# Kernel tuning notes

Hardware: AMD Instinct MI355X
Metric: run time of the kernel (lower is better)

The kernel has to match this reference:

```python
import jax, jax.numpy as jnp
import numpy as np

B = 2048   # number of samples; acts as seq_len for the (S,N,E) transformer
DIN = 768
D = 512    # hidden_dim
H = 8      # nheads
HD = D // H
L = 3      # encoder layers
P = 40     # num_prototypes
Q = D // 4 # 128, projected feature dim
EPS = 1e-5


def setup_inputs() -> dict:
    key = jax.random.key(0)
    ks = jax.random.split(key, 22)
    s = 0.02
    rn = lambda k, shape: jax.random.normal(k, shape, jnp.float32) * s
    return {
        "x": jax.random.normal(ks[0], (B, DIN), jnp.float32),
        "reduce_w": rn(ks[1], (D, DIN)), "reduce_b": rn(ks[2], (D,)),
        "in_w": rn(ks[3], (L, 3 * D, D)), "in_b": rn(ks[4], (L, 3 * D)),
        "out_w": rn(ks[5], (L, D, D)), "out_b": rn(ks[6], (L, D)),
        "ff1_w": rn(ks[7], (L, D, D)), "ff1_b": rn(ks[8], (L, D)),
        "ff2_w": rn(ks[9], (L, D, D)), "ff2_b": rn(ks[10], (L, D)),
        "ln1_w": jnp.ones((L, D), jnp.float32), "ln1_b": jnp.zeros((L, D), jnp.float32),
        "ln2_w": jnp.ones((L, D), jnp.float32), "ln2_b": jnp.zeros((L, D), jnp.float32),
        "mlp_w1": rn(ks[11], (D, D)), "mlp_b1": rn(ks[12], (D,)),
        "mlp_w2": rn(ks[13], (D, D)), "mlp_b2": rn(ks[14], (D,)),
        "mlp_w3": rn(ks[15], (Q, D)), "mlp_b3": rn(ks[16], (Q,)),
        "highlights": jax.random.normal(ks[17], (P, Q), jnp.float32),
        "negatives": jax.random.normal(ks[18], (P, Q), jnp.float32),
    }


def _inorm(x):
    # InstanceNorm1d (affine=False) on a 2D tensor: per-row normalize over last dim
    m = x.mean(-1, keepdims=True)
    v = ((x - m) ** 2).mean(-1, keepdims=True)  # biased variance, matches torch
    return (x - m) * jax.lax.rsqrt(v + EPS)


def _ln(x, w, b):
    m = x.mean(-1, keepdims=True)
    v = ((x - m) ** 2).mean(-1, keepdims=True)
    return (x - m) * jax.lax.rsqrt(v + EPS) * w + b


def _cdist(a, cb):
    # euclidean distances [B,P]
    d2 = (a * a).sum(-1, keepdims=True) + (cb * cb).sum(-1) - 2.0 * a @ cb.T
    return jnp.sqrt(jnp.maximum(d2, 0.0))


def reference(x, reduce_w, reduce_b, in_w, in_b, out_w, out_b,
              ff1_w, ff1_b, ff2_w, ff2_b, ln1_w, ln1_b, ln2_w, ln2_b,
              mlp_w1, mlp_b1, mlp_w2, mlp_b2, mlp_w3, mlp_b3,
              highlights, negatives):
    feat0 = _inorm(x @ reduce_w.T + reduce_b)  # [B,D]

    # TransformerEncoder, post-norm, relu FFN, dropout off (eval).
    # Input is (seq=B, batch=1, D) -> attention across all B rows.
    feat = feat0
    scale = 1.0 / np.sqrt(HD)
    for i in range(L):
        qkv = feat @ in_w[i].T + in_b[i]           # [B,3D]
        q, k, v = jnp.split(qkv, 3, axis=-1)
        q = q.reshape(B, H, HD)
        k = k.reshape(B, H, HD)
        v = v.reshape(B, H, HD)
        scores = jnp.einsum('ihd,jhd->hij', q, k) * scale  # [H,B,B]
        attn = jax.nn.softmax(scores, axis=-1)
        ctx = jnp.einsum('hij,jhd->ihd', attn, v).reshape(B, D)
        attn_out = ctx @ out_w[i].T + out_b[i]
        feat = _ln(feat + attn_out, ln1_w[i], ln1_b[i])
        ff = jax.nn.relu(feat @ ff1_w[i].T + ff1_b[i]) @ ff2_w[i].T + ff2_b[i]
        feat = _ln(feat + ff, ln2_w[i], ln2_b[i])

    feat = feat0 + _inorm(feat)

    # MLP 512 -> 512 -> 512 -> 128 (relu on all but last)
    feat = jax.nn.relu(feat @ mlp_w1.T + mlp_b1)
    feat = jax.nn.relu(feat @ mlp_w2.T + mlp_b2)
    feat = feat @ mlp_w3.T + mlp_b3
    feat = _inorm(feat)  # [B,Q]

    positive_dist = _cdist(feat, highlights).min(-1)
    negative_dist = _cdist(feat, negatives).min(-1)
    logits = jnp.stack([-negative_dist, -positive_dist], axis=-1)  # [B,2]
    return logits
```

## Files before the change

### kernel.cpp

```cpp
#include <hip/hip_runtime.h>
#include <math.h>
#include <cstddef>

#define EPS 1e-5f

typedef __attribute__((ext_vector_type(8))) short bf16x8;
typedef __attribute__((ext_vector_type(4))) float f32x4;

__device__ __forceinline__ float wave_sum(float v) {
#pragma unroll
  for (int o = 32; o > 0; o >>= 1) v += __shfl_xor(v, o, 64);
  return v;
}

__device__ __forceinline__ unsigned short f2b(float f) {
  union { float f; unsigned int u; } v; v.f = f;
  unsigned int r = (v.u + 0x7FFFu + ((v.u >> 16) & 1u)) >> 16;
  return (unsigned short)r;
}
__device__ __forceinline__ float b2f(unsigned short u) {
  union { unsigned int u; float f; } v; v.u = ((unsigned int)u) << 16;
  return v.f;
}

struct WConvArgs {
  const float* src[8];
  unsigned short* dst[8];
  int n[8];
};
__global__ __launch_bounds__(256) void conv_w(WConvArgs a) {
  const int arr = blockIdx.y;
  const int i = (blockIdx.x * 256 + threadIdx.x) * 4;
  if (i >= a.n[arr]) return;
  const float4 f = *(const float4*)(a.src[arr] + i);
  unsigned short t[4] = {f2b(f.x), f2b(f.y), f2b(f.z), f2b(f.w)};
  unsigned short* d = a.dst[arr] + i;
  *(ushort2*)d = *(ushort2*)&t[0];
  *(ushort2*)(d + 2) = *(ushort2*)&t[2];
}

template <int RELU, int AF32, int OUT_F32, int OUT_BF16, int MERGE>
__global__ __launch_bounds__(256) void gemm32(
    const void* __restrict__ Aptr, const float* __restrict__ pmp,
    const unsigned short* __restrict__ W, const float* __restrict__ bias,
    float* __restrict__ Cf, unsigned short* __restrict__ Cb,
    int M, int N, int K) {
  __shared__ __align__(16) unsigned short As[2][32][72];
  __shared__ __align__(16) unsigned short Ws[2][64][72];
  const int tid = threadIdx.x;
  const int wid = tid >> 6, lane = tid & 63;
  const int ln = lane & 15, quad = lane >> 4;
  const int m0 = blockIdx.x * 32, n0 = blockIdx.y * 64;
  const int arow = tid >> 3, aseg = tid & 7;
  const int wrow = tid >> 2, wseg = tid & 3;
  const int KS = K >> 6;

  bf16x8 ra;
  float4 ra32[2];
  bf16x8 rwb0, rwb1;
  bf16x8 rp0, rp1;
  float rl0, rl1;

  auto load_tile = [&](int ks) {
    const int k0 = ks * 64;
    if (MERGE) {
      const int h = ks;
      const int row = m0 + arow;
      const size_t b0 = (size_t)(h * 2048 + row);
      const size_t b1 = (size_t)((8 + h) * 2048 + row);
      rl0 = pmp[b0]; rl1 = pmp[b1];
      rp0 = *(const bf16x8*)((const unsigned short*)Aptr + b0 * 64 + aseg * 8);
      rp1 = *(const bf16x8*)((const unsigned short*)Aptr + b1 * 64 + aseg * 8);
    } else if (AF32) {
      const float* ap = (const float*)Aptr + (size_t)(m0 + arow) * K + k0 + aseg * 8;
      ra32[0] = *(const float4*)ap;
      ra32[1] = *(const float4*)(ap + 4);
    } else {
      ra = *(const bf16x8*)((const unsigned short*)Aptr +
                            (size_t)(m0 + arow) * K + k0 + aseg * 8);
    }
    const unsigned short* wp = W + (size_t)(n0 + wrow) * K + k0 + wseg * 16;
    rwb0 = *(const bf16x8*)wp;
    rwb1 = *(const bf16x8*)(wp + 8);
  };

  auto store_tile = [&](int buf) {
    if (MERGE) {
      float inv = 1.f / (rl0 + rl1);
      unsigned short ta[8];
#pragma unroll
      for (int j = 0; j < 8; ++j)
        ta[j] = f2b(inv * (b2f((unsigned short)rp0[j]) +
                           b2f((unsigned short)rp1[j])));
      *(bf16x8*)&As[buf][arow][aseg * 8] = *(const bf16x8*)&ta[0];
    } else if (AF32) {
      unsigned short ta[8];
      ta[0] = f2b(ra32[0].x); ta[1] = f2b(ra32[0].y);
      ta[2] = f2b(ra32[0].z); ta[3] = f2b(ra32[0].w);
      ta[4] = f2b(ra32[1].x); ta[5] = f2b(ra32[1].y);
      ta[6] = f2b(ra32[1].z); ta[7] = f2b(ra32[1].w);
      *(bf16x8*)&As[buf][arow][aseg * 8] = *(const bf16x8*)&ta[0];
    } else {
      *(bf16x8*)&As[buf][arow][aseg * 8] = ra;
    }
    *(bf16x8*)&Ws[buf][wrow][wseg * 16] = rwb0;
    *(bf16x8*)&Ws[buf][wrow][wseg * 16 + 8] = rwb1;
  };

  f32x4 acc[2];
  acc[0] = (f32x4){0.f, 0.f, 0.f, 0.f};
  acc[1] = (f32x4){0.f, 0.f, 0.f, 0.f};

  const int mrow = (wid & 1) * 16, nh = wid >> 1;

  load_tile(0);
  store_tile(0);
  __syncthreads();

#pragma unroll 1
  for (int ks = 0; ks < KS; ++ks) {
    const int cur = ks & 1;
    if (ks + 1 < KS) load_tile(ks + 1);
#pragma unroll
    for (int kc = 0; kc < 2; ++kc) {
      bf16x8 af = *(const bf16x8*)&As[cur][mrow + ln][kc * 32 + quad * 8];
#pragma unroll
      for (int nt = 0; nt < 2; ++nt) {
        bf16x8 wf = *(const bf16x8*)&Ws[cur][nh * 32 + nt * 16 + ln][kc * 32 + quad * 8];
        acc[nt] = __builtin_amdgcn_mfma_f32_16x16x32_bf16(af, wf, acc[nt], 0, 0, 0);
      }
    }
    if (ks + 1 < KS) store_tile(cur ^ 1);
    __syncthreads();
  }

  const int gm = m0 + mrow + quad * 4;
#pragma unroll
  for (int nt = 0; nt < 2; ++nt) {
    const int gn = n0 + nh * 32 + nt * 16 + ln;
    float bv = bias[gn];
#pragma unroll
    for (int r = 0; r < 4; ++r) {
      float v = acc[nt][r] + bv;
      if (RELU) v = fmaxf(v, 0.f);
      if (OUT_F32) Cf[(size_t)(gm + r) * N + gn] = v;
      if (OUT_BF16) Cb[(size_t)(gm + r) * N + gn] = f2b(v);
    }
  }
}

__global__ __launch_bounds__(256) void flash_attn6(
    const unsigned short* __restrict__ qkv, float* __restrict__ pm,
    unsigned short* __restrict__ po) {
  __shared__ __align__(16) unsigned short Ks[2][64][72];
  __shared__ __align__(16) unsigned short Vt[2][64][72];
  __shared__ __align__(16) unsigned short Ps[64][72];
  const int qt = blockIdx.x, h = blockIdx.y, sp = blockIdx.z;
  const int tid = threadIdx.x;
  const int wid = tid >> 6, lane = tid & 63;
  const int ln = lane & 15, quad = lane >> 4;
  const int wq0 = wid * 16;

  bf16x8 aq[2];
  {
    const unsigned short* qp =
        qkv + (size_t)(qt * 64 + wq0 + ln) * 1536 + h * 64 + quad * 8;
    aq[0] = *(const bf16x8*)qp;
    aq[1] = *(const bf16x8*)(qp + 32);
  }

  const int key = tid >> 2, seg = tid & 3;
  bf16x8 rk0, rk1;
  unsigned short tv[16];

  auto load_kv = [&](int t) {
    const int g = sp * 16 + t;
    const unsigned short* kr =
        qkv + (size_t)(g * 64 + key) * 1536 + 512 + h * 64 + seg * 16;
    rk0 = *(const bf16x8*)kr;
    rk1 = *(const bf16x8*)(kr + 8);
#pragma unroll
    for (int j = 0; j < 16; ++j)
      tv[j] = qkv[(size_t)(g * 64 + wid * 16 + j) * 1536 + 1024 + h * 64 + lane];
  };
  auto store_kv = [&](int buf) {
    *(bf16x8*)&Ks[buf][key][seg * 16] = rk0;
    *(bf16x8*)&Ks[buf][key][seg * 16 + 8] = rk1;
    *(bf16x8*)&Vt[buf][lane][wid * 16] = *(const bf16x8*)&tv[0];
    *(bf16x8*)&Vt[buf][lane][wid * 16 + 8] = *(const bf16x8*)&tv[8];
  };

  float l_r[4] = {0.f, 0.f, 0.f, 0.f};
  f32x4 acc_o[4];
#pragma unroll
  for (int nt = 0; nt < 4; ++nt) acc_o[nt] = (f32x4){0.f, 0.f, 0.f, 0.f};

  load_kv(0);
  store_kv(0);
  __syncthreads();

#pragma unroll 1
  for (int t = 0; t < 16; ++t) {
    const int cur = t & 1;
    if (t + 1 < 16) load_kv(t + 1);

    f32x4 s_acc[4];
#pragma unroll
    for (int nt = 0; nt < 4; ++nt) s_acc[nt] = (f32x4){0.f, 0.f, 0.f, 0.f};
#pragma unroll
    for (int nt = 0; nt < 4; ++nt) {
      bf16x8 kf0 = *(const bf16x8*)&Ks[cur][nt * 16 + ln][quad * 8];
      bf16x8 kf1 = *(const bf16x8*)&Ks[cur][nt * 16 + ln][32 + quad * 8];
      s_acc[nt] = __builtin_amdgcn_mfma_f32_16x16x32_bf16(aq[0], kf0, s_acc[nt], 0, 0, 0);
      s_acc[nt] = __builtin_amdgcn_mfma_f32_16x16x32_bf16(aq[1], kf1, s_acc[nt], 0, 0, 0);
    }

#pragma unroll
    for (int nt = 0; nt < 4; ++nt) {
#pragma unroll
      for (int r = 0; r < 4; ++r) {
        float p = __expf(s_acc[nt][r] * 0.125f);
        l_r[r] += p;
        Ps[wq0 + quad * 4 + r][nt * 16 + ln] = f2b(p);
      }
    }

#pragma unroll
    for (int kc = 0; kc < 2; ++kc) {
      bf16x8 pf = *(const bf16x8*)&Ps[wq0 + ln][kc * 32 + quad * 8];
#pragma unroll
      for (int nt = 0; nt < 4; ++nt) {
        bf16x8 vf = *(const bf16x8*)&Vt[cur][nt * 16 + ln][kc * 32 + quad * 8];
        acc_o[nt] = __builtin_amdgcn_mfma_f32_16x16x32_bf16(pf, vf, acc_o[nt], 0, 0, 0);
      }
    }
    if (t + 1 < 16) store_kv(cur ^ 1);
    __syncthreads();
  }

  const size_t base = (size_t)((sp * 8 + h) * 2048 + qt * 64);
#pragma unroll
  for (int r = 0; r < 4; ++r) {
    float l = l_r[r];
    l += __shfl_xor(l, 1, 64);
    l += __shfl_xor(l, 2, 64);
    l += __shfl_xor(l, 4, 64);
    l += __shfl_xor(l, 8, 64);
    const size_t row = base + wq0 + quad * 4 + r;
    if (ln == 0) pm[row] = l;
#pragma unroll
    for (int nt = 0; nt < 4; ++nt)
      po[row * 64 + nt * 16 + ln] = f2b(acc_o[nt][r]);
  }
}

__global__ __launch_bounds__(256) void inorm512(float* __restrict__ dst,
                                                unsigned short* __restrict__ dstb,
                                                const float* __restrict__ src) {
  const int row = blockIdx.x * 4 + (threadIdx.x >> 6);
  const int lane = threadIdx.x & 63;
  const float4* s = (const float4*)(src + (size_t)row * 512);
  float4 a = s[lane], b = s[lane + 64];
  float sum = a.x + a.y + a.z + a.w + b.x + b.y + b.z + b.w;
  float mean = wave_sum(sum) * (1.f / 512.f);
  float vs = (a.x - mean) * (a.x - mean) + (a.y - mean) * (a.y - mean) +
             (a.z - mean) * (a.z - mean) + (a.w - mean) * (a.w - mean) +
             (b.x - mean) * (b.x - mean) + (b.y - mean) * (b.y - mean) +
             (b.z - mean) * (b.z - mean) + (b.w - mean) * (b.w - mean);
  float rs = rsqrtf(wave_sum(vs) * (1.f / 512.f) + EPS);
  float4 oa, obv;
  oa.x = (a.x - mean) * rs; oa.y = (a.y - mean) * rs;
  oa.z = (a.z - mean) * rs; oa.w = (a.w - mean) * rs;
  obv.x = (b.x - mean) * rs; obv.y = (b.y - mean) * rs;
  obv.z = (b.z - mean) * rs; obv.w = (b.w - mean) * rs;
  float4* d = (float4*)(dst + (size_t)row * 512);
  d[lane] = oa; d[lane + 64] = obv;
  unsigned short* db = dstb + (size_t)row * 512;
  unsigned short t0[4] = {f2b(oa.x), f2b(oa.y), f2b(oa.z), f2b(oa.w)};
  unsigned short t1[4] = {f2b(obv.x), f2b(obv.y), f2b(obv.z), f2b(obv.w)};
  *(ushort2*)&db[lane * 4] = *(ushort2*)&t0[0];
  *(ushort2*)&db[lane * 4 + 2] = *(ushort2*)&t0[2];
  *(ushort2*)&db[256 + lane * 4] = *(ushort2*)&t1[0];
  *(ushort2*)&db[256 + lane * 4 + 2] = *(ushort2*)&t1[2];
}

__global__ __launch_bounds__(256) void ln_res(float* __restrict__ dst,
                                              unsigned short* __restrict__ dstb,
                                              const float* __restrict__ xsrc,
                                              const float* __restrict__ delta,
                                              const float* __restrict__ w,
                                              const float* __restrict__ bb) {
  const int row = blockIdx.x * 4 + (threadIdx.x >> 6);
  const int lane = threadIdx.x & 63;
  const float4* xs = (const float4*)(xsrc + (size_t)row * 512);
  const float4* dl = (const float4*)(delta + (size_t)row * 512);
  float4 a = xs[lane], b = xs[lane + 64];
  float4 da = dl[lane], db4 = dl[lane + 64];
  a.x += da.x; a.y += da.y; a.z += da.z; a.w += da.w;
  b.x += db4.x; b.y += db4.y; b.z += db4.z; b.w += db4.w;
  float sum = a.x + a.y + a.z + a.w + b.x + b.y + b.z + b.w;
  float mean = wave_sum(sum) * (1.f / 512.f);
  float vs = (a.x - mean) * (a.x - mean) + (a.y - mean) * (a.y - mean) +
             (a.z - mean) * (a.z - mean) + (a.w - mean) * (a.w - mean) +
             (b.x - mean) * (b.x - mean) + (b.y - mean) * (b.y - mean) +
             (b.z - mean) * (b.z - mean) + (b.w - mean) * (b.w - mean);
  float rs = rsqrtf(wave_sum(vs) * (1.f / 512.f) + EPS);
  float4 wa = ((const float4*)w)[lane], wb = ((const float4*)w)[lane + 64];
  float4 ba = ((const float4*)bb)[lane], bbv = ((const float4*)bb)[lane + 64];
  float4 oa, ob2;
  oa.x = (a.x - mean) * rs * wa.x + ba.x; oa.y = (a.y - mean) * rs * wa.y + ba.y;
  oa.z = (a.z - mean) * rs * wa.z + ba.z; oa.w = (a.w - mean) * rs * wa.w + ba.w;
  ob2.x = (b.x - mean) * rs * wb.x + bbv.x; ob2.y = (b.y - mean) * rs * wb.y + bbv.y;
  ob2.z = (b.z - mean) * rs * wb.z + bbv.z; ob2.w = (b.w - mean) * rs * wb.w + bbv.w;
  float4* d = (float4*)(dst + (size_t)row * 512);
  d[lane] = oa; d[lane + 64] = ob2;
  unsigned short* dbp = dstb + (size_t)row * 512;
  unsigned short t0[4] = {f2b(oa.x), f2b(oa.y), f2b(oa.z), f2b(oa.w)};
  unsigned short t1[4] = {f2b(ob2.x), f2b(ob2.y), f2b(ob2.z), f2b(ob2.w)};
  *(ushort2*)&dbp[lane * 4] = *(ushort2*)&t0[0];
  *(ushort2*)&dbp[lane * 4 + 2] = *(ushort2*)&t0[2];
  *(ushort2*)&dbp[256 + lane * 4] = *(ushort2*)&t1[0];
  *(ushort2*)&dbp[256 + lane * 4 + 2] = *(ushort2*)&t1[2];
}

__global__ __launch_bounds__(256) void add_inorm(float* __restrict__ feat,
                                                 unsigned short* __restrict__ featb,
                                                 const float* __restrict__ feat0) {
  const int row = blockIdx.x * 4 + (threadIdx.x >> 6);
  const int lane = threadIdx.x & 63;
  float4* f = (float4*)(feat + (size_t)row * 512);
  const float4* f0 = (const float4*)(feat0 + (size_t)row * 512);
  float4 a = f[lane], b = f[lane + 64];
  float sum = a.x + a.y + a.z + a.w + b.x + b.y + b.z + b.w;
  float mean = wave_sum(sum) * (1.f / 512.f);
  float vs = (a.x - mean) * (a.x - mean) + (a.y - mean) * (a.y - mean) +
             (a.z - mean) * (a.z - mean) + (a.w - mean) * (a.w - mean) +
             (b.x - mean) * (b.x - mean) + (b.y - mean) * (b.y - mean) +
             (b.z - mean) * (b.z - mean) + (b.w - mean) * (b.w - mean);
  float rs = rsqrtf(wave_sum(vs) * (1.f / 512.f) + EPS);
  float4 za = f0[lane], zb = f0[lane + 64];
  float4 oa, ob2;
  oa.x = za.x + (a.x - mean) * rs; oa.y = za.y + (a.y - mean) * rs;
  oa.z = za.z + (a.z - mean) * rs; oa.w = za.w + (a.w - mean) * rs;
  ob2.x = zb.x + (b.x - mean) * rs; ob2.y = zb.y + (b.y - mean) * rs;
  ob2.z = zb.z + (b.z - mean) * rs; ob2.w = zb.w + (b.w - mean) * rs;
  f[lane] = oa; f[lane + 64] = ob2;
  unsigned short* dbp = featb + (size_t)row * 512;
  unsigned short t0[4] = {f2b(oa.x), f2b(oa.y), f2b(oa.z), f2b(oa.w)};
  unsigned short t1[4] = {f2b(ob2.x), f2b(ob2.y), f2b(ob2.z), f2b(ob2.w)};
  *(ushort2*)&dbp[lane * 4] = *(ushort2*)&t0[0];
  *(ushort2*)&dbp[lane * 4 + 2] = *(ushort2*)&t0[2];
  *(ushort2*)&dbp[256 + lane * 4] = *(ushort2*)&t1[0];
  *(ushort2*)&dbp[256 + lane * 4 + 2] = *(ushort2*)&t1[2];
}

__global__ __launch_bounds__(256) void dist2(const float* __restrict__ fq,
                                             const float* __restrict__ hi,
                                             const float* __restrict__ ne,
                                             float* __restrict__ out) {
  const int row = blockIdx.x * 4 + (threadIdx.x >> 6);
  const int lane = threadIdx.x & 63;
  float f0 = fq[(size_t)row * 128 + lane];
  float f1 = fq[(size_t)row * 128 + 64 + lane];
  float mean = wave_sum(f0 + f1) * (1.f / 128.f);
  float vs = (f0 - mean) * (f0 - mean) + (f1 - mean) * (f1 - mean);
  float rs = rsqrtf(wave_sum(vs) * (1.f / 128.f) + EPS);
  f0 = (f0 - mean) * rs;
  f1 = (f1 - mean) * rs;
  float mp = 1e30f, mn = 1e30f;
  for (int p = 0; p < 40; ++p) {
    float h0 = hi[p * 128 + lane], h1 = hi[p * 128 + 64 + lane];
    float d0 = f0 - h0, d1 = f1 - h1;
    float d2 = wave_sum(d0 * d0 + d1 * d1);
    mp = fminf(mp, d2);
    float n0 = ne[p * 128 + lane], n1 = ne[p * 128 + 64 + lane];
    d0 = f0 - n0; d1 = f1 - n1;
    d2 = wave_sum(d0 * d0 + d1 * d1);
    mn = fminf(mn, d2);
  }
  if (lane == 0) {
    out[row * 2 + 0] = -sqrtf(mn);
    out[row * 2 + 1] = -sqrtf(mp);
  }
}

extern "C" void kernel_launch(void* const* d_in, const int* in_sizes, int n_in,
                              void* d_out, int out_size, void* d_ws, size_t ws_size,
                              hipStream_t stream) {
  const float* x        = (const float*)d_in[0];
  const float* reduce_w = (const float*)d_in[1];
  const float* reduce_b = (const float*)d_in[2];
  const float* in_w     = (const float*)d_in[3];
  const float* in_b     = (const float*)d_in[4];
  const float* out_w    = (const float*)d_in[5];
  const float* out_b    = (const float*)d_in[6];
  const float* ff1_w    = (const float*)d_in[7];
  const float* ff1_b    = (const float*)d_in[8];
  const float* ff2_w    = (const float*)d_in[9];
  const float* ff2_b    = (const float*)d_in[10];
  const float* ln1_w    = (const float*)d_in[11];
  const float* ln1_b    = (const float*)d_in[12];
  const float* ln2_w    = (const float*)d_in[13];
  const float* ln2_b    = (const float*)d_in[14];
  const float* mlp_w1   = (const float*)d_in[15];
  const float* mlp_b1   = (const float*)d_in[16];
  const float* mlp_w2   = (const float*)d_in[17];
  const float* mlp_b2   = (const float*)d_in[18];
  const float* mlp_w3   = (const float*)d_in[19];
  const float* mlp_b3   = (const float*)d_in[20];
  const float* hi       = (const float*)d_in[21];
  const float* ne       = (const float*)d_in[22];
  float* out = (float*)d_out;
  float* ws = (float*)d_ws;

  const size_t MD = (size_t)2048 * 512;
  float* feat0_f = ws;
  float* feat_f  = ws + MD;
  float* tmp_f   = ws + 2 * MD;
  float* pm      = ws + 3 * MD;
  unsigned short* u = (unsigned short*)(ws + 3 * MD + 32768);
  unsigned short* qkv_b   = u;
  unsigned short* feat0_b = u + 3 * MD;
  unsigned short* feat_b  = u + 4 * MD;
  unsigned short* relu_b  = u + 5 * MD;
  unsigned short* po_b    = u + 6 * MD;
  unsigned short* relu2_b = qkv_b;
  float* featq_f = tmp_f;

  unsigned short* wb = u + 8 * MD;
  unsigned short* reduce_wb = wb;
  unsigned short* in_wb     = wb + 393216;
  unsigned short* out_wb    = in_wb + 2359296;
  unsigned short* ff1_wb    = out_wb + 786432;
  unsigned short* ff2_wb    = ff1_wb + 786432;
  unsigned short* mlp_w1b   = ff2_wb + 786432;
  unsigned short* mlp_w2b   = mlp_w1b + 262144;
  unsigned short* mlp_w3b   = mlp_w2b + 262144;

  dim3 blk(256);
  WConvArgs wa;
  wa.src[0] = reduce_w; wa.dst[0] = reduce_wb; wa.n[0] = 393216;
  wa.src[1] = in_w;     wa.dst[1] = in_wb;     wa.n[1] = 2359296;
  wa.src[2] = out_w;    wa.dst[2] = out_wb;    wa.n[2] = 786432;
  wa.src[3] = ff1_w;    wa.dst[3] = ff1_wb;    wa.n[3] = 786432;
  wa.src[4] = ff2_w;    wa.dst[4] = ff2_wb;    wa.n[4] = 786432;
  wa.src[5] = mlp_w1;   wa.dst[5] = mlp_w1b;   wa.n[5] = 262144;
  wa.src[6] = mlp_w2;   wa.dst[6] = mlp_w2b;   wa.n[6] = 262144;
  wa.src[7] = mlp_w3;   wa.dst[7] = mlp_w3b;   wa.n[7] = 65536;
  conv_w<<<dim3(2304, 8), blk, 0, stream>>>(wa);

  gemm32<0, 1, 1, 0, 0><<<dim3(64, 8), blk, 0, stream>>>(
      x, nullptr, reduce_wb, reduce_b, feat0_f, nullptr, 2048, 512, 768);
  inorm512<<<512, blk, 0, stream>>>(feat0_f, feat0_b, feat0_f);

  for (int i = 0; i < 3; ++i) {
    const float* fin_f = (i == 0) ? feat0_f : feat_f;
    const unsigned short* fin_b = (i == 0) ? feat0_b : feat_b;
    gemm32<0, 0, 0, 1, 0><<<dim3(64, 24), blk, 0, stream>>>(
        fin_b, nullptr, in_wb + (size_t)i * 1536 * 512, in_b + i * 1536,
        nullptr, qkv_b, 2048, 1536, 512);
    flash_attn6<<<dim3(32, 8, 2), blk, 0, stream>>>(qkv_b, pm, po_b);
    gemm32<0, 0, 1, 0, 1><<<dim3(64, 8), blk, 0, stream>>>(
        po_b, pm, out_wb + (size_t)i * 512 * 512, out_b + i * 512,
        tmp_f, nullptr, 2048, 512, 512);
    ln_res<<<512, blk, 0, stream>>>(feat_f, feat_b, fin_f, tmp_f,
                                    ln1_w + i * 512, ln1_b + i * 512);
    gemm32<1, 0, 0, 1, 0><<<dim3(64, 8), blk, 0, stream>>>(
        feat_b, nullptr, ff1_wb + (size_t)i * 512 * 512, ff1_b + i * 512,
        nullptr, relu_b, 2048, 512, 512);
    gemm32<0, 0, 1, 0, 0><<<dim3(64, 8), blk, 0, stream>>>(
        relu_b, nullptr, ff2_wb + (size_t)i * 512 * 512, ff2_b + i * 512,
        tmp_f, nullptr, 2048, 512, 512);
    ln_res<<<512, blk, 0, stream>>>(feat_f, feat_b, feat_f, tmp_f,
                                    ln2_w + i * 512, ln2_b + i * 512);
  }

  add_inorm<<<512, blk, 0, stream>>>(feat_f, feat_b, feat0_f);
  gemm32<1, 0, 0, 1, 0><<<dim3(64, 8), blk, 0, stream>>>(
      feat_b, nullptr, mlp_w1b, mlp_b1, nullptr, relu_b, 2048, 512, 512);
  gemm32<1, 0, 0, 1, 0><<<dim3(64, 8), blk, 0, stream>>>(
      relu_b, nullptr, mlp_w2b, mlp_b2, nullptr, relu2_b, 2048, 512, 512);
  gemm32<0, 0, 1, 0, 0><<<dim3(64, 2), blk, 0, stream>>>(
      relu2_b, nullptr, mlp_w3b, mlp_b3, featq_f, nullptr, 2048, 128, 512);
  dist2<<<512, blk, 0, stream>>>(featq_f, hi, ne, out);
}
```

Before: 373.1 us.

## Split attention keys four ways, fold Q scaling and residual adds into GEMMs

The flash attention grid grows from 2 to 4 key splits, each processing 8 key tiles. The K/V shared buffers become single-buffered with an extra barrier per tile, and the out-projection merge step now sums four partials. The 1/sqrt(d) query scaling moves into the QKV GEMM epilogue. The residual additions move into the out-proj and FF2 GEMM epilogues, so the layernorm kernels read one tensor instead of two. This aims to raise attention occupancy across CUs and cut memory traffic, at the cost of more partial-result traffic and extra synchronization inside the attention loop.

```diff
diff --git a/kernel.cpp b/kernel.cpp
--- a/kernel.cpp
+++ b/kernel.cpp
@@ -39,12 +39,13 @@
   *(ushort2*)(d + 2) = *(ushort2*)&t[2];
 }
 
-template <int RELU, int AF32, int OUT_F32, int OUT_BF16, int MERGE>
+template <int RELU, int AF32, int OUT_F32, int OUT_BF16, int MERGE, int RESID,
+          int SCALEQ>
 __global__ __launch_bounds__(256) void gemm32(
     const void* __restrict__ Aptr, const float* __restrict__ pmp,
     const unsigned short* __restrict__ W, const float* __restrict__ bias,
-    float* __restrict__ Cf, unsigned short* __restrict__ Cb,
-    int M, int N, int K) {
+    const float* __restrict__ Rf, float* __restrict__ Cf,
+    unsigned short* __restrict__ Cb, int M, int N, int K) {
   __shared__ __align__(16) unsigned short As[2][32][72];
   __shared__ __align__(16) unsigned short Ws[2][64][72];
   const int tid = threadIdx.x;
@@ -58,19 +59,21 @@
   bf16x8 ra;
   float4 ra32[2];
   bf16x8 rwb0, rwb1;
-  bf16x8 rp0, rp1;
-  float rl0, rl1;
+  bf16x8 rp[4];
+  float rl;
 
   auto load_tile = [&](int ks) {
     const int k0 = ks * 64;
     if (MERGE) {
       const int h = ks;
       const int row = m0 + arow;
-      const size_t b0 = (size_t)(h * 2048 + row);
-      const size_t b1 = (size_t)((8 + h) * 2048 + row);
-      rl0 = pmp[b0]; rl1 = pmp[b1];
-      rp0 = *(const bf16x8*)((const unsigned short*)Aptr + b0 * 64 + aseg * 8);
-      rp1 = *(const bf16x8*)((const unsigned short*)Aptr + b1 * 64 + aseg * 8);
+      rl = 0.f;
+#pragma unroll
+      for (int s = 0; s < 4; ++s) {
+        const size_t b = (size_t)((s * 8 + h) * 2048 + row);
+        rl += pmp[b];
+        rp[s] = *(const bf16x8*)((const unsigned short*)Aptr + b * 64 + aseg * 8);
+      }
     } else if (AF32) {
       const float* ap = (const float*)Aptr + (size_t)(m0 + arow) * K + k0 + aseg * 8;
       ra32[0] = *(const float4*)ap;
@@ -86,12 +89,14 @@
 
   auto store_tile = [&](int buf) {
     if (MERGE) {
-      float inv = 1.f / (rl0 + rl1);
+      float inv = 1.f / rl;
       unsigned short ta[8];
 #pragma unroll
-      for (int j = 0; j < 8; ++j)
-        ta[j] = f2b(inv * (b2f((unsigned short)rp0[j]) +
-                           b2f((unsigned short)rp1[j])));
+      for (int j = 0; j < 8; ++j) {
+        float s = b2f((unsigned short)rp[0][j]) + b2f((unsigned short)rp[1][j]) +
+                  b2f((unsigned short)rp[2][j]) + b2f((unsigned short)rp[3][j]);
+        ta[j] = f2b(inv * s);
+      }
       *(bf16x8*)&As[buf][arow][aseg * 8] = *(const bf16x8*)&ta[0];
     } else if (AF32) {
       unsigned short ta[8];
@@ -135,6 +140,7 @@
   }
 
   const int gm = m0 + mrow + quad * 4;
+  const float qs = (SCALEQ && n0 < 512) ? 0.125f : 1.f;
 #pragma unroll
   for (int nt = 0; nt < 2; ++nt) {
     const int gn = n0 + nh * 32 + nt * 16 + ln;
@@ -142,18 +148,20 @@
 #pragma unroll
     for (int r = 0; r < 4; ++r) {
       float v = acc[nt][r] + bv;
+      if (SCALEQ) v *= qs;
       if (RELU) v = fmaxf(v, 0.f);
+      if (RESID) v += Rf[(size_t)(gm + r) * N + gn];
       if (OUT_F32) Cf[(size_t)(gm + r) * N + gn] = v;
       if (OUT_BF16) Cb[(size_t)(gm + r) * N + gn] = f2b(v);
     }
   }
 }
 
-__global__ __launch_bounds__(256) void flash_attn6(
+__global__ __launch_bounds__(256) void flash_attn7(
     const unsigned short* __restrict__ qkv, float* __restrict__ pm,
     unsigned short* __restrict__ po) {
-  __shared__ __align__(16) unsigned short Ks[2][64][72];
-  __shared__ __align__(16) unsigned short Vt[2][64][72];
+  __shared__ __align__(16) unsigned short Ks[64][72];
+  __shared__ __align__(16) unsigned short Vt[64][72];
   __shared__ __align__(16) unsigned short Ps[64][72];
   const int qt = blockIdx.x, h = blockIdx.y, sp = blockIdx.z;
   const int tid = threadIdx.x;
@@ -174,7 +182,7 @@
   unsigned short tv[16];
 
   auto load_kv = [&](int t) {
-    const int g = sp * 16 + t;
+    const int g = sp * 8 + t;
     const unsigned short* kr =
         qkv + (size_t)(g * 64 + key) * 1536 + 512 + h * 64 + seg * 16;
     rk0 = *(const bf16x8*)kr;
@@ -183,11 +191,11 @@
     for (int j = 0; j < 16; ++j)
       tv[j] = qkv[(size_t)(g * 64 + wid * 16 + j) * 1536 + 1024 + h * 64 + lane];
   };
-  auto store_kv = [&](int buf) {
-    *(bf16x8*)&Ks[buf][key][seg * 16] = rk0;
-    *(bf16x8*)&Ks[buf][key][seg * 16 + 8] = rk1;
-    *(bf16x8*)&Vt[buf][lane][wid * 16] = *(const bf16x8*)&tv[0];
-    *(bf16x8*)&Vt[buf][lane][wid * 16 + 8] = *(const bf16x8*)&tv[8];
+  auto store_kv = [&]() {
+    *(bf16x8*)&Ks[key][seg * 16] = rk0;
+    *(bf16x8*)&Ks[key][seg * 16 + 8] = rk1;
+    *(bf16x8*)&Vt[lane][wid * 16] = *(const bf16x8*)&tv[0];
+    *(bf16x8*)&Vt[lane][wid * 16 + 8] = *(const bf16x8*)&tv[8];
   };
 
   float l_r[4] = {0.f, 0.f, 0.f, 0.f};
@@ -196,21 +204,20 @@
   for (int nt = 0; nt < 4; ++nt) acc_o[nt] = (f32x4){0.f, 0.f, 0.f, 0.f};
 
   load_kv(0);
-  store_kv(0);
+  store_kv();
   __syncthreads();
 
 #pragma unroll 1
-  for (int t = 0; t < 16; ++t) {
-    const int cur = t & 1;
-    if (t + 1 < 16) load_kv(t + 1);
+  for (int t = 0; t < 8; ++t) {
+    if (t + 1 < 8) load_kv(t + 1);
 
     f32x4 s_acc[4];
 #pragma unroll
     for (int nt = 0; nt < 4; ++nt) s_acc[nt] = (f32x4){0.f, 0.f, 0.f, 0.f};
 #pragma unroll
     for (int nt = 0; nt < 4; ++nt) {
-      bf16x8 kf0 = *(const bf16x8*)&Ks[cur][nt * 16 + ln][quad * 8];
-      bf16x8 kf1 = *(const bf16x8*)&Ks[cur][nt * 16 + ln][32 + quad * 8];
+      bf16x8 kf0 = *(const bf16x8*)&Ks[nt * 16 + ln][quad * 8];
+      bf16x8 kf1 = *(const bf16x8*)&Ks[nt * 16 + ln][32 + quad * 8];
       s_acc[nt] = __builtin_amdgcn_mfma_f32_16x16x32_bf16(aq[0], kf0, s_acc[nt], 0, 0, 0);
       s_acc[nt] = __builtin_amdgcn_mfma_f32_16x16x32_bf16(aq[1], kf1, s_acc[nt], 0, 0, 0);
     }
@@ -219,7 +226,7 @@
     for (int nt = 0; nt < 4; ++nt) {
 #pragma unroll
       for (int r = 0; r < 4; ++r) {
-        float p = __expf(s_acc[nt][r] * 0.125f);
+        float p = __expf(s_acc[nt][r]);
         l_r[r] += p;
         Ps[wq0 + quad * 4 + r][nt * 16 + ln] = f2b(p);
       }
@@ -230,12 +237,15 @@
       bf16x8 pf = *(const bf16x8*)&Ps[wq0 + ln][kc * 32 + quad * 8];
 #pragma unroll
       for (int nt = 0; nt < 4; ++nt) {
-        bf16x8 vf = *(const bf16x8*)&Vt[cur][nt * 16 + ln][kc * 32 + quad * 8];
+        bf16x8 vf = *(const bf16x8*)&Vt[nt * 16 + ln][kc * 32 + quad * 8];
         acc_o[nt] = __builtin_amdgcn_mfma_f32_16x16x32_bf16(pf, vf, acc_o[nt], 0, 0, 0);
       }
     }
-    if (t + 1 < 16) store_kv(cur ^ 1);
     __syncthreads();
+    if (t + 1 < 8) {
+      store_kv();
+      __syncthreads();
+    }
   }
 
   const size_t base = (size_t)((sp * 8 + h) * 2048 + qt * 64);
@@ -284,20 +294,15 @@
   *(ushort2*)&db[256 + lane * 4 + 2] = *(ushort2*)&t1[2];
 }
 
-__global__ __launch_bounds__(256) void ln_res(float* __restrict__ dst,
-                                              unsigned short* __restrict__ dstb,
-                                              const float* __restrict__ xsrc,
-                                              const float* __restrict__ delta,
-                                              const float* __restrict__ w,
-                                              const float* __restrict__ bb) {
+__global__ __launch_bounds__(256) void ln_res2(float* __restrict__ dst,
+                                               unsigned short* __restrict__ dstb,
+                                               const float* __restrict__ src,
+                                               const float* __restrict__ w,
+                                               const float* __restrict__ bb) {
   const int row = blockIdx.x * 4 + (threadIdx.x >> 6);
   const int lane = threadIdx.x & 63;
-  const float4* xs = (const float4*)(xsrc + (size_t)row * 512);
-  const float4* dl = (const float4*)(delta + (size_t)row * 512);
+  const float4* xs = (const float4*)(src + (size_t)row * 512);
   float4 a = xs[lane], b = xs[lane + 64];
-  float4 da = dl[lane], db4 = dl[lane + 64];
-  a.x += da.x; a.y += da.y; a.z += da.z; a.w += da.w;
-  b.x += db4.x; b.y += db4.y; b.z += db4.z; b.w += db4.w;
   float sum = a.x + a.y + a.z + a.w + b.x + b.y + b.z + b.w;
   float mean = wave_sum(sum) * (1.f / 512.f);
   float vs = (a.x - mean) * (a.x - mean) + (a.y - mean) * (a.y - mean) +
@@ -418,7 +423,7 @@
   float* feat_f  = ws + MD;
   float* tmp_f   = ws + 2 * MD;
   float* pm      = ws + 3 * MD;
-  unsigned short* u = (unsigned short*)(ws + 3 * MD + 32768);
+  unsigned short* u = (unsigned short*)(ws + 3 * MD + 65536);
   unsigned short* qkv_b   = u;
   unsigned short* feat0_b = u + 3 * MD;
   unsigned short* feat_b  = u + 4 * MD;
@@ -427,7 +432,7 @@
   unsigned short* relu2_b = qkv_b;
   float* featq_f = tmp_f;
 
-  unsigned short* wb = u + 8 * MD;
+  unsigned short* wb = u + 10 * MD;
   unsigned short* reduce_wb = wb;
   unsigned short* in_wb     = wb + 393216;
   unsigned short* out_wb    = in_wb + 2359296;
@@ -449,38 +454,38 @@
   wa.src[7] = mlp_w3;   wa.dst[7] = mlp_w3b;   wa.n[7] = 65536;
   conv_w<<<dim3(2304, 8), blk, 0, stream>>>(wa);
 
-  gemm32<0, 1, 1, 0, 0><<<dim3(64, 8), blk, 0, stream>>>(
-      x, nullptr, reduce_wb, reduce_b, feat0_f, nullptr, 2048, 512, 768);
+  gemm32<0, 1, 1, 0, 0, 0, 0><<<dim3(64, 8), blk, 0, stream>>>(
+      x, nullptr, reduce_wb, reduce_b, nullptr, feat0_f, nullptr, 2048, 512, 768);
   inorm512<<<512, blk, 0, stream>>>(feat0_f, feat0_b, feat0_f);
 
   for (int i = 0; i < 3; ++i) {
     const float* fin_f = (i == 0) ? feat0_f : feat_f;
     const unsigned short* fin_b = (i == 0) ? feat0_b : feat_b;
-    gemm32<0, 0, 0, 1, 0><<<dim3(64, 24), blk, 0, stream>>>(
+    gemm32<0, 0, 0, 1, 0, 0, 1><<<dim3(64, 24), blk, 0, stream>>>(
         fin_b, nullptr, in_wb + (size_t)i * 1536 * 512, in_b + i * 1536,
-        nullptr, qkv_b, 2048, 1536, 512);
-    flash_attn6<<<dim3(32, 8, 2), blk, 0, stream>>>(qkv_b, pm, po_b);
-    gemm32<0, 0, 1, 0, 1><<<dim3(64, 8), blk, 0, stream>>>(
+        nullptr, nullptr, qkv_b, 2048, 1536, 512);
+    flash_attn7<<<dim3(32, 8, 4), blk, 0, stream>>>(qkv_b, pm, po_b);
+    gemm32<0, 0, 1, 0, 1, 1, 0><<<dim3(64, 8), blk, 0, stream>>>(
         po_b, pm, out_wb + (size_t)i * 512 * 512, out_b + i * 512,
-        tmp_f, nullptr, 2048, 512, 512);
-    ln_res<<<512, blk, 0, stream>>>(feat_f, feat_b, fin_f, tmp_f,
-                                    ln1_w + i * 512, ln1_b + i * 512);
-    gemm32<1, 0, 0, 1, 0><<<dim3(64, 8), blk, 0, stream>>>(
+        fin_f, tmp_f, nullptr, 2048, 512, 512);
+    ln_res2<<<512, blk, 0, stream>>>(feat_f, feat_b, tmp_f,
+                                     ln1_w + i * 512, ln1_b + i * 512);
+    gemm32<1, 0, 0, 1, 0, 0, 0><<<dim3(64, 8), blk, 0, stream>>>(
         feat_b, nullptr, ff1_wb + (size_t)i * 512 * 512, ff1_b + i * 512,
-        nullptr, relu_b, 2048, 512, 512);
-    gemm32<0, 0, 1, 0, 0><<<dim3(64, 8), blk, 0, stream>>>(
+        nullptr, nullptr, relu_b, 2048, 512, 512);
+    gemm32<0, 0, 1, 0, 0, 1, 0><<<dim3(64, 8), blk, 0, stream>>>(
         relu_b, nullptr, ff2_wb + (size_t)i * 512 * 512, ff2_b + i * 512,
-        tmp_f, nullptr, 2048, 512, 512);
-    ln_res<<<512, blk, 0, stream>>>(feat_f, feat_b, feat_f, tmp_f,
-                                    ln2_w + i * 512, ln2_b + i * 512);
+        feat_f, tmp_f, nullptr, 2048, 512, 512);
+    ln_res2<<<512, blk, 0, stream>>>(feat_f, feat_b, tmp_f,
+                                     ln2_w + i * 512, ln2_b + i * 512);
   }
 
   add_inorm<<<512, blk, 0, stream>>>(feat_f, feat_b, feat0_f);
-  gemm32<1, 0, 0, 1, 0><<<dim3(64, 8), blk, 0, stream>>>(
-      feat_b, nullptr, mlp_w1b, mlp_b1, nullptr, relu_b, 2048, 512, 512);
-  gemm32<1, 0, 0, 1, 0><<<dim3(64, 8), blk, 0, stream>>>(
-      relu_b, nullptr, mlp_w2b, mlp_b2, nullptr, relu2_b, 2048, 512, 512);
-  gemm32<0, 0, 1, 0, 0><<<dim3(64, 2), blk, 0, stream>>>(
-      relu2_b, nullptr, mlp_w3b, mlp_b3, featq_f, nullptr, 2048, 128, 512);
+  gemm32<1, 0, 0, 1, 0, 0, 0><<<dim3(64, 8), blk, 0, stream>>>(
+      feat_b, nullptr, mlp_w1b, mlp_b1, nullptr, nullptr, relu_b, 2048, 512, 512);
+  gemm32<1, 0, 0, 1, 0, 0, 0><<<dim3(64, 8), blk, 0, stream>>>(
+      relu_b, nullptr, mlp_w2b, mlp_b2, nullptr, nullptr, relu2_b, 2048, 512, 512);
+  gemm32<0, 0, 1, 0, 0, 0, 0><<<dim3(64, 2), blk, 0, stream>>>(
+      relu2_b, nullptr, mlp_w3b, mlp_b3, nullptr, featq_f, nullptr, 2048, 128, 512);
   dist2<<<512, blk, 0, stream>>>(featq_f, hi, ne, out);
 }
```

Result: faster. 365.0 us (-2.2%).
